# Kernel tuning notes

Hardware: AMD Instinct MI355X
Metric: run time of the kernel (lower is better)

Reference implementation:

```python
import jax, jax.numpy as jnp
import numpy as np

B, S, E = 4, 2048, 512
Q, FFN = 8, 2048


def setup_inputs() -> dict:
    key = jax.random.key(0)
    k_x, k_th, k_w1, k_w2 = jax.random.split(key, 4)
    x = jax.random.normal(k_x, (B, S, E), dtype=jnp.float32)
    # trainable RY angles, one per wire
    theta = jax.random.normal(k_th, (Q,), dtype=jnp.float32)
    W1 = jax.random.normal(k_w1, (Q, FFN), dtype=jnp.float32) / np.sqrt(Q)
    b1 = jnp.zeros((FFN,), dtype=jnp.float32)
    W2 = jax.random.normal(k_w2, (FFN, E), dtype=jnp.float32) / np.sqrt(FFN)
    b2 = jnp.zeros((E,), dtype=jnp.float32)
    return {"x": x, "theta": theta, "W1": W1, "b1": b1, "W2": W2, "b2": b2}


def reference(x, theta, W1, b1, W2, b2):
    # Quantum circuit: |0> -> RX(x_i) -> RY(theta_i) -> <Z> per wire.
    # No entangling gates, so the 8-qubit state factorizes; simulate each
    # qubit's 2 complex amplitudes, batched over all tokens & wires at once.
    n_wires = theta.shape[0]
    xq = x[..., :n_wires]                     # encoder uses input_idx 0..7: [B,S,Q]
    # RX(x)|0> = cos(x/2)|0> - i sin(x/2)|1>
    a = jnp.cos(xq * 0.5).astype(jnp.complex64)
    b = (-1j) * jnp.sin(xq * 0.5).astype(jnp.complex64)
    # RY(theta) = [[c,-s],[s,c]], c=cos(theta/2), s=sin(theta/2)
    c = jnp.cos(theta * 0.5).astype(jnp.complex64)
    s = jnp.sin(theta * 0.5).astype(jnp.complex64)
    a2 = c * a - s * b
    b2_ = s * a + c * b
    # <Z> = |amp0|^2 - |amp1|^2  -> [B,S,Q]
    z = (jnp.abs(a2) ** 2 - jnp.abs(b2_) ** 2).astype(x.dtype)
    # dropout is identity at inference
    h = jax.nn.relu(jnp.einsum('bsq,qf->bsf', z, W1) + b1)
    return jnp.einsum('bsf,fe->bse', h, W2) + b2
```

## Files before the change

### kernel.cpp

```cpp
#include <hip/hip_runtime.h>
#include <hip/hip_bf16.h>

typedef __bf16 bf16_t;
typedef __bf16 bf16x4 __attribute__((ext_vector_type(4)));
typedef __bf16 bf16x8 __attribute__((ext_vector_type(8)));
typedef float f32x4 __attribute__((ext_vector_type(4)));

#define M_TOT 8192
#define N_TOT 512
#define K_TOT 2048
#define E_TOT 512
#define NSEG_HALF 16

__device__ __forceinline__ bf16x8 zero8() {
    bf16x8 v;
#pragma unroll
    for (int i = 0; i < 8; ++i) v[i] = (bf16_t)0.0f;
    return v;
}

__global__ __launch_bounds__(256)
void prep4_kernel(const float* __restrict__ x,
                  const float* __restrict__ theta,
                  const float* __restrict__ W1,
                  const float* __restrict__ b1,
                  const float* __restrict__ W2,
                  bf16_t* __restrict__ W2t,
                  bf16_t* __restrict__ zb,
                  bf16_t* __restrict__ W1p)
{
    const int b = blockIdx.x;
    if (b < 256) {
        __shared__ bf16_t T[64][66];
        const int k0 = (b >> 3) * 64;
        const int n0 = (b & 7) * 64;
        const int kl = threadIdx.x >> 4;
        const int n4 = threadIdx.x & 15;
#pragma unroll
        for (int i = 0; i < 4; ++i) {
            int k = kl + i * 16;
            float4 v = *(const float4*)(W2 + (size_t)(k0 + k) * N_TOT + n0 + n4 * 4);
            T[n4 * 4 + 0][k] = (bf16_t)v.x;
            T[n4 * 4 + 1][k] = (bf16_t)v.y;
            T[n4 * 4 + 2][k] = (bf16_t)v.z;
            T[n4 * 4 + 3][k] = (bf16_t)v.w;
        }
        __syncthreads();
        const int nl = threadIdx.x >> 4;
        const int k4 = threadIdx.x & 15;
#pragma unroll
        for (int i = 0; i < 4; ++i) {
            int n = nl + i * 16;
            bf16x4 v;
            v[0] = T[n][k4 * 4 + 0];
            v[1] = T[n][k4 * 4 + 1];
            v[2] = T[n][k4 * 4 + 2];
            v[3] = T[n][k4 * 4 + 3];
            *(bf16x4*)(W2t + (size_t)(n0 + n) * K_TOT + k0 + k4 * 4) = v;
        }
    } else if (b < 288) {
        const int m = (b - 256) * 256 + threadIdx.x;
        float4 x0 = *(const float4*)(x + (size_t)m * E_TOT);
        float4 x1 = *(const float4*)(x + (size_t)m * E_TOT + 4);
        float xs[8] = {x0.x, x0.y, x0.z, x0.w, x1.x, x1.y, x1.z, x1.w};
        bf16x8 lo;
#pragma unroll
        for (int q = 0; q < 8; ++q)
            lo[q] = (bf16_t)(__builtin_cosf(theta[q]) * __builtin_cosf(xs[q]));
        bf16x8 hi = zero8();
        hi[0] = (bf16_t)1.0f;
        *(bf16x8*)(zb + (size_t)m * 16)     = lo;
        *(bf16x8*)(zb + (size_t)m * 16 + 8) = hi;
    } else {
        const int d  = (b - 288) * 256 + threadIdx.x;
        const int c  = d >> 5;
        const int dd = d & 31;
        const int p  = dd >> 4;
        const int rr = dd & 15;
        const int f  = c * 32 + ((rr >> 2) << 3) + (p << 2) + (rr & 3);
        bf16x8 lo;
#pragma unroll
        for (int q = 0; q < 8; ++q)
            lo[q] = (bf16_t)W1[(size_t)q * K_TOT + f];
        bf16x8 hi = zero8();
        hi[0] = (bf16_t)b1[f];
        *(bf16x8*)(W1p + (size_t)d * 16)     = lo;
        *(bf16x8*)(W1p + (size_t)d * 16 + 8) = hi;
    }
}

__device__ __forceinline__ void stage_B(const bf16_t* __restrict__ W2t,
                                        bf16_t* dst_buf, int n_base, int k0,
                                        int wl, int l) {
#pragma unroll
    for (int j = 0; j < 4; ++j) {
        int s = wl * 64 + l + j * 128;
        int n = (s >> 3) & 63;
        int g = (s & 7) ^ (n & 7);
        const bf16_t* src = W2t + (size_t)(n_base + n) * K_TOT + k0 + g * 8;
        bf16_t* ldst = dst_buf + (size_t)(wl * 64 + j * 128) * 8;
        __builtin_amdgcn_global_load_lds(
            (const __attribute__((address_space(1))) unsigned int*)src,
            (__attribute__((address_space(3))) unsigned int*)ldst,
            16, 0, 0);
    }
}

__device__ __forceinline__ void load_wf(const bf16_t* __restrict__ W1p, int k0,
                                        int l15, int lq, bf16x8 wf[4]) {
#pragma unroll
    for (int i = 0; i < 4; ++i) wf[i] = zero8();
    if (lq < 2) {
        const int base = (k0 >> 5) * 2;
#pragma unroll
        for (int i = 0; i < 4; ++i)
            wf[i] = *(const bf16x8*)(W1p + (size_t)((base + i) * 16 + l15) * 16 + lq * 8);
    }
}

__device__ __forceinline__ void compute_tile(const bf16_t* Bb, const bf16x8 wf[4],
                                             const bf16x8 zfrag[2],
                                             int l15, int lq,
                                             f32x4 acc[2][4]) {
    bf16x8 bfr[2][4];
#pragma unroll
    for (int c = 0; c < 2; ++c)
#pragma unroll
        for (int nt = 0; nt < 4; ++nt) {
            int r = nt * 16 + l15;
            int s = (c * 4 + lq) ^ (r & 7);
            bfr[c][nt] = *(const bf16x8*)(Bb + r * 64 + s * 8);
        }

    bf16x8 af[2][2];
#pragma unroll
    for (int mt = 0; mt < 2; ++mt)
#pragma unroll
        for (int c = 0; c < 2; ++c) {
            f32x4 h0 = (f32x4){0.f, 0.f, 0.f, 0.f};
            f32x4 h1 = (f32x4){0.f, 0.f, 0.f, 0.f};
            h0 = __builtin_amdgcn_mfma_f32_16x16x32_bf16(wf[c * 2 + 0], zfrag[mt], h0, 0, 0, 0);
            h1 = __builtin_amdgcn_mfma_f32_16x16x32_bf16(wf[c * 2 + 1], zfrag[mt], h1, 0, 0, 0);
            bf16x8 a;
#pragma unroll
            for (int r = 0; r < 4; ++r) {
                a[r]     = (bf16_t)fmaxf(h0[r], 0.f);
                a[r + 4] = (bf16_t)fmaxf(h1[r], 0.f);
            }
            af[mt][c] = a;
        }

#pragma unroll
    for (int c = 0; c < 2; ++c)
#pragma unroll
        for (int mt = 0; mt < 2; ++mt)
#pragma unroll
            for (int nt = 0; nt < 4; ++nt)
                acc[mt][nt] = __builtin_amdgcn_mfma_f32_16x16x32_bf16(
                    af[mt][c], bfr[c][nt], acc[mt][nt], 0, 0, 0);
}

__global__ __launch_bounds__(256, 4)
void ffq_gemm_kernel(const bf16_t* __restrict__ zb,
                     const bf16_t* __restrict__ W1p,
                     const bf16_t* __restrict__ W2t,
                     const float* __restrict__ b2,
                     float* __restrict__ out)
{
    __shared__ bf16_t Blds[2][2][64 * 64];

    const int t  = threadIdx.x;
    const int w  = t >> 6, l = t & 63;
    const int ks = w >> 1;
    const int wl = w & 1;
    const int m_base = blockIdx.y * 64;
    const int n_base = blockIdx.x * 64;
    const int l15 = l & 15, lq = l >> 4;
    const int k_base = ks * 1024;

    bf16x8 zfrag[2];
#pragma unroll
    for (int mt = 0; mt < 2; ++mt) {
        zfrag[mt] = zero8();
        if (lq < 2)
            zfrag[mt] = *(const bf16x8*)(zb + (size_t)(m_base + wl * 32 + mt * 16 + l15) * 16 + lq * 8);
    }

    f32x4 acc[2][4];
#pragma unroll
    for (int mt = 0; mt < 2; ++mt)
#pragma unroll
        for (int nt = 0; nt < 4; ++nt)
            acc[mt][nt] = (f32x4){0.f, 0.f, 0.f, 0.f};

    stage_B(W2t, Blds[ks][0], n_base, k_base, wl, l);

    for (int s = 0; s < NSEG_HALF; ++s) {
        const int cur = s & 1;
        __syncthreads();
        if (s + 1 < NSEG_HALF)
            stage_B(W2t, Blds[ks][1 - cur], n_base, k_base + (s + 1) * 64, wl, l);

        bf16x8 wf[4];
        load_wf(W1p, k_base + s * 64, l15, lq, wf);
        compute_tile(Blds[ks][cur], wf, zfrag, l15, lq, acc);
    }

    __syncthreads();
    float* F = (float*)&Blds[0][0][0];
    if (ks == 1) {
#pragma unroll
        for (int mt = 0; mt < 2; ++mt)
#pragma unroll
            for (int nt = 0; nt < 4; ++nt) {
                int idx = ((wl * 2 + mt) * 4 + nt) * 64 + l;
                *(f32x4*)(F + (size_t)idx * 4) = acc[mt][nt];
            }
    }
    __syncthreads();
    if (ks == 0) {
#pragma unroll
        for (int nt = 0; nt < 4; ++nt) {
            int col = n_base + nt * 16 + l15;
            float bias = b2[col];
#pragma unroll
            for (int mt = 0; mt < 2; ++mt) {
                int idx = ((wl * 2 + mt) * 4 + nt) * 64 + l;
                f32x4 part = *(const f32x4*)(F + (size_t)idx * 4);
#pragma unroll
                for (int r = 0; r < 4; ++r) {
                    int row = m_base + wl * 32 + mt * 16 + lq * 4 + r;
                    out[(size_t)row * N_TOT + col] = acc[mt][nt][r] + part[r] + bias;
                }
            }
        }
    }
}

extern "C" void kernel_launch(void* const* d_in, const int* in_sizes, int n_in,
                              void* d_out, int out_size, void* d_ws, size_t ws_size,
                              hipStream_t stream) {
    const float* x     = (const float*)d_in[0];
    const float* theta = (const float*)d_in[1];
    const float* W1    = (const float*)d_in[2];
    const float* b1    = (const float*)d_in[3];
    const float* W2    = (const float*)d_in[4];
    const float* b2    = (const float*)d_in[5];
    float* out = (float*)d_out;

    const size_t W2T_BYTES = (size_t)N_TOT * K_TOT * sizeof(bf16_t);
    const size_t ZB_BYTES  = (size_t)M_TOT * 16 * sizeof(bf16_t);

    bf16_t* W2t = (bf16_t*)d_ws;
    bf16_t* zb  = (bf16_t*)((char*)d_ws + W2T_BYTES);
    bf16_t* W1p = (bf16_t*)((char*)d_ws + W2T_BYTES + ZB_BYTES);

    prep4_kernel<<<296, 256, 0, stream>>>(x, theta, W1, b1, W2, W2t, zb, W1p);

    dim3 grid(N_TOT / 64, M_TOT / 64);
    ffq_gemm_kernel<<<grid, 256, 0, stream>>>(zb, W1p, W2t, b2, out);
}
```

Measured before the change: 102.9 us.

## Pre-pack W2 into MFMA fragment order and read B directly from global

```diff
diff --git a/kernel.cpp b/kernel.cpp
--- a/kernel.cpp
+++ b/kernel.cpp
@@ -25,7 +25,7 @@
                   const float* __restrict__ W1,
                   const float* __restrict__ b1,
                   const float* __restrict__ W2,
-                  bf16_t* __restrict__ W2t,
+                  bf16_t* __restrict__ W2f,
                   bf16_t* __restrict__ zb,
                   bf16_t* __restrict__ W1p)
 {
@@ -46,17 +46,19 @@
             T[n4 * 4 + 3][k] = (bf16_t)v.w;
         }
         __syncthreads();
-        const int nl = threadIdx.x >> 4;
-        const int k4 = threadIdx.x & 15;
-#pragma unroll
-        for (int i = 0; i < 4; ++i) {
-            int n = nl + i * 16;
-            bf16x4 v;
-            v[0] = T[n][k4 * 4 + 0];
-            v[1] = T[n][k4 * 4 + 1];
-            v[2] = T[n][k4 * 4 + 2];
-            v[3] = T[n][k4 * 4 + 3];
-            *(bf16x4*)(W2t + (size_t)(n0 + n) * K_TOT + k0 + k4 * 4) = v;
+        const size_t base = (size_t)((b & 7) * 32 + (b >> 3)) * 4096;
+#pragma unroll
+        for (int i = 0; i < 2; ++i) {
+            int ci = threadIdx.x + i * 256;
+            int c  = ci >> 8;
+            int nt = (ci >> 6) & 3;
+            int l  = ci & 63;
+            int nl = nt * 16 + (l & 15);
+            int kk = (c * 4 + (l >> 4)) * 8;
+            bf16x8 v;
+#pragma unroll
+            for (int j = 0; j < 8; ++j) v[j] = T[nl][kk + j];
+            *(bf16x8*)(W2f + base + (size_t)ci * 8) = v;
         }
     } else if (b < 288) {
         const int m = (b - 256) * 256 + threadIdx.x;
@@ -89,23 +91,6 @@
     }
 }
 
-__device__ __forceinline__ void stage_B(const bf16_t* __restrict__ W2t,
-                                        bf16_t* dst_buf, int n_base, int k0,
-                                        int wl, int l) {
-#pragma unroll
-    for (int j = 0; j < 4; ++j) {
-        int s = wl * 64 + l + j * 128;
-        int n = (s >> 3) & 63;
-        int g = (s & 7) ^ (n & 7);
-        const bf16_t* src = W2t + (size_t)(n_base + n) * K_TOT + k0 + g * 8;
-        bf16_t* ldst = dst_buf + (size_t)(wl * 64 + j * 128) * 8;
-        __builtin_amdgcn_global_load_lds(
-            (const __attribute__((address_space(1))) unsigned int*)src,
-            (__attribute__((address_space(3))) unsigned int*)ldst,
-            16, 0, 0);
-    }
-}
-
 __device__ __forceinline__ void load_wf(const bf16_t* __restrict__ W1p, int k0,
                                         int l15, int lq, bf16x8 wf[4]) {
 #pragma unroll
@@ -118,19 +103,17 @@
     }
 }
 
-__device__ __forceinline__ void compute_tile(const bf16_t* Bb, const bf16x8 wf[4],
+__device__ __forceinline__ void compute_tile(const bf16_t* __restrict__ tb,
+                                             const bf16x8 wf[4],
                                              const bf16x8 zfrag[2],
-                                             int l15, int lq,
+                                             int l,
                                              f32x4 acc[2][4]) {
     bf16x8 bfr[2][4];
 #pragma unroll
     for (int c = 0; c < 2; ++c)
 #pragma unroll
-        for (int nt = 0; nt < 4; ++nt) {
-            int r = nt * 16 + l15;
-            int s = (c * 4 + lq) ^ (r & 7);
-            bfr[c][nt] = *(const bf16x8*)(Bb + r * 64 + s * 8);
-        }
+        for (int nt = 0; nt < 4; ++nt)
+            bfr[c][nt] = *(const bf16x8*)(tb + (size_t)(c * 256 + nt * 64 + l) * 8);
 
     bf16x8 af[2][2];
 #pragma unroll
@@ -163,18 +146,19 @@
 __global__ __launch_bounds__(256, 4)
 void ffq_gemm_kernel(const bf16_t* __restrict__ zb,
                      const bf16_t* __restrict__ W1p,
-                     const bf16_t* __restrict__ W2t,
+                     const bf16_t* __restrict__ W2f,
                      const float* __restrict__ b2,
                      float* __restrict__ out)
 {
-    __shared__ bf16_t Blds[2][2][64 * 64];
+    __shared__ float F[4096];
 
     const int t  = threadIdx.x;
     const int w  = t >> 6, l = t & 63;
     const int ks = w >> 1;
     const int wl = w & 1;
     const int m_base = blockIdx.y * 64;
-    const int n_base = blockIdx.x * 64;
+    const int n_blk  = blockIdx.x;
+    const int n_base = n_blk * 64;
     const int l15 = l & 15, lq = l >> 4;
     const int k_base = ks * 1024;
 
@@ -193,21 +177,15 @@
         for (int nt = 0; nt < 4; ++nt)
             acc[mt][nt] = (f32x4){0.f, 0.f, 0.f, 0.f};
 
-    stage_B(W2t, Blds[ks][0], n_base, k_base, wl, l);
+    const bf16_t* tb = W2f + (size_t)(n_blk * 32 + ks * 16) * 4096;
 
     for (int s = 0; s < NSEG_HALF; ++s) {
-        const int cur = s & 1;
-        __syncthreads();
-        if (s + 1 < NSEG_HALF)
-            stage_B(W2t, Blds[ks][1 - cur], n_base, k_base + (s + 1) * 64, wl, l);
-
         bf16x8 wf[4];
         load_wf(W1p, k_base + s * 64, l15, lq, wf);
-        compute_tile(Blds[ks][cur], wf, zfrag, l15, lq, acc);
+        compute_tile(tb + (size_t)s * 4096, wf, zfrag, l, acc);
     }
 
     __syncthreads();
-    float* F = (float*)&Blds[0][0][0];
     if (ks == 1) {
 #pragma unroll
         for (int mt = 0; mt < 2; ++mt)
@@ -248,15 +226,15 @@
     const float* b2    = (const float*)d_in[5];
     float* out = (float*)d_out;
 
-    const size_t W2T_BYTES = (size_t)N_TOT * K_TOT * sizeof(bf16_t);
+    const size_t W2F_BYTES = (size_t)N_TOT * K_TOT * sizeof(bf16_t);
     const size_t ZB_BYTES  = (size_t)M_TOT * 16 * sizeof(bf16_t);
 
-    bf16_t* W2t = (bf16_t*)d_ws;
-    bf16_t* zb  = (bf16_t*)((char*)d_ws + W2T_BYTES);
-    bf16_t* W1p = (bf16_t*)((char*)d_ws + W2T_BYTES + ZB_BYTES);
-
-    prep4_kernel<<<296, 256, 0, stream>>>(x, theta, W1, b1, W2, W2t, zb, W1p);
+    bf16_t* W2f = (bf16_t*)d_ws;
+    bf16_t* zb  = (bf16_t*)((char*)d_ws + W2F_BYTES);
+    bf16_t* W1p = (bf16_t*)((char*)d_ws + W2F_BYTES + ZB_BYTES);
+
+    prep4_kernel<<<296, 256, 0, stream>>>(x, theta, W1, b1, W2, W2f, zb, W1p);
 
     dim3 grid(N_TOT / 64, M_TOT / 64);
-    ffq_gemm_kernel<<<grid, 256, 0, stream>>>(zb, W1p, W2t, b2, out);
-}
+    ffq_gemm_kernel<<<grid, 256, 0, stream>>>(zb, W1p, W2f, b2, out);
+}
```

Result: no change. 103.4 us (+0.5%).
